# Performance work log

Hardware: AMD Instinct MI355X
Metric: run time of the kernel (lower is better)

The kernel has to match this reference:

```python
import jax, jax.numpy as jnp
import numpy as np

EPS = 1e-6

def _ln(x, g, b):
    m = jnp.mean(x, axis=-1, keepdims=True)
    v = jnp.mean(jnp.square(x - m), axis=-1, keepdims=True)
    return (x - m) * jax.lax.rsqrt(v + EPS) * g + b

def setup_inputs() -> dict:
    key = jax.random.key(0)
    ks = jax.random.split(key, 8)
    B, T, D, K = 512, 1024, 64, 16
    return {
        "z": jax.random.normal(ks[0], (B, T, D), jnp.float32),
        "prototypes": jax.random.normal(ks[1], (K, D), jnp.float32),
        "alphas": jax.random.normal(ks[2], (T, D), jnp.float32),
        "b_bias": jax.random.normal(ks[3], (D,), jnp.float32),
        "W": jax.random.normal(ks[4], (D, D), jnp.float32) / np.sqrt(D),
        "Wb": jax.random.normal(ks[5], (D,), jnp.float32) * 0.02,
        "ln_gamma": jnp.ones((5, D), jnp.float32),
        "ln_beta": jnp.zeros((5, D), jnp.float32),
        "beta_seq": jax.random.normal(ks[6], (K, D), jnp.float32) / np.sqrt(D),
    }

def reference(z, prototypes, alphas, b_bias, W, Wb, ln_gamma, ln_beta, beta_seq):
    # z: [B,T,D], prototypes: [K,D], alphas: [T,D]
    D = z.shape[-1]
    scale = 1.0 / jnp.sqrt(jnp.asarray(D, z.dtype))

    # --- intention_clustering: p_{k|i} ---
    zn = _ln(z, ln_gamma[0], ln_beta[0])                      # [B,T,D]
    pn = _ln(prototypes, ln_gamma[1], ln_beta[1])             # [K,D]
    scores_k = jnp.einsum('btd,kd->btk', zn, pn) * scale      # [B,T,K]
    p_k_i = jax.nn.softmax(scores_k, axis=-1)                 # normalize over intents K

    # --- intention_weighting: p_i ---
    k_ = _ln(alphas + z, ln_gamma[2], ln_beta[2])             # [B,T,D]
    k = k_ + jnp.einsum('btd,de->bte', k_, W) + Wb            # residual Dense
    q = _ln(alphas[-1] + z[:, -1] + b_bias, ln_gamma[3], ln_beta[3])  # [B,D] last-position query
    scores_t = jnp.einsum('btd,bd->bt', k, q) * scale         # [B,T]
    p_i = jax.nn.softmax(scores_t, axis=1)                    # normalize over positions T

    # --- intention_aggr ---
    w = p_k_i * p_i[..., None]                                # [B,T,K]
    out = jnp.einsum('btk,btd->bkd', w, z)                    # [B,K,D]
    return _ln(beta_seq + out, ln_gamma[4], ln_beta[4])       # [B,K,D]
```

## Files before the change

### kernel.cpp

```cpp
#include <hip/hip_runtime.h>
#include <math.h>

#define EPSF   1e-6f
#define SCALE  0.125f
#define NEG_HUGE -3.402823466e38f

#define PW_STRIDE 4104

__device__ __forceinline__ float rs_nr(float x) {
    float r = rsqrtf(x);
    return r * (1.5f - 0.5f * x * r * r);
}

__device__ __forceinline__ float dot4(float4 a, float4 b) {
    return fmaf(a.x, b.x, fmaf(a.y, b.y, fmaf(a.z, b.z, a.w * b.w)));
}

__device__ __forceinline__ float finish_token(
    float sz, float szz, float sa, float saa, float da,
    const float* dk, const float* s_sGP, const float* s_BP,
    float sG2Q, float TQc, float* sk, float* se)
{
    float m   = sz  * (1.f / 64.f);
    float var = szz * (1.f / 64.f) - m * m;
    float rs  = rs_nr(var + EPSF);
    float ma   = sa  * (1.f / 64.f);
    float vara = saa * (1.f / 64.f) - ma * ma;
    float rsa  = rs_nr(vara + EPSF);

    float st = (rsa * (da - ma * sG2Q) + TQc) * SCALE;

    float mx = NEG_HUGE;
#pragma unroll
    for (int k = 0; k < 16; ++k) {
        float s = (rs * (dk[k] - m * s_sGP[k]) + s_BP[k]) * SCALE;
        sk[k] = s;
        mx = fmaxf(mx, s);
    }
    float s0 = 0.f;
#pragma unroll
    for (int k = 0; k < 16; ++k) { sk[k] = __expf(sk[k] - mx); s0 += sk[k]; }
    *se = s0;
    return st;
}

extern "C" __global__ __launch_bounds__(512, 4)
void disent_encoder_kernel(const float* __restrict__ z,
                           const float* __restrict__ proto,
                           const float* __restrict__ alphas,
                           const float* __restrict__ b_bias,
                           const float* __restrict__ W,
                           const float* __restrict__ Wb,
                           const float* __restrict__ lng,
                           const float* __restrict__ lnb,
                           const float* __restrict__ beta_seq,
                           float* __restrict__ out)
{
    const int b    = blockIdx.x;
    const int tid  = threadIdx.x;
    const int lane = tid & 63;
    const int wid  = tid >> 6;

    __shared__ __align__(16) float s_pw[4 * PW_STRIDE];
    __shared__ __align__(16) float s_GP[16 * 64];
    __shared__ __align__(16) float s_G2Q[64];
    __shared__ float s_sGP[16];
    __shared__ float s_BP[16];
    __shared__ float s_red[12];
    __shared__ float s_c[2];

    const float* zb = z + (size_t)b * 1024 * 64;

    if (wid == 0) {
        int d = lane;
        float a = alphas[1023 * 64 + d] + zb[1023 * 64 + d] + b_bias[d];
        float s1 = a, s2 = a * a;
#pragma unroll
        for (int off = 32; off >= 1; off >>= 1) {
            s1 += __shfl_xor(s1, off);
            s2 += __shfl_xor(s2, off);
        }
        float m  = s1 * (1.f / 64.f);
        float v  = s2 * (1.f / 64.f) - m * m;
        float rs = rs_nr(v + EPSF);
        float qd = fmaf((a - m) * rs, lng[3*64 + d], lnb[3*64 + d]);
        float s = 0.f;
#pragma unroll 4
        for (int eq = 0; eq < 16; ++eq) {
            float4 w4 = *(const float4*)&W[d*64 + eq*4];
            s = fmaf(w4.x, __shfl(qd, 4*eq+0),
                fmaf(w4.y, __shfl(qd, 4*eq+1),
                fmaf(w4.z, __shfl(qd, 4*eq+2),
                fmaf(w4.w, __shfl(qd, 4*eq+3), s))));
        }
        float qpp  = qd + s;
        float G2Qd = lng[2*64 + d] * qpp;
        s_G2Q[d] = G2Qd;
        float r1 = G2Qd;
        float r2 = fmaf(lnb[2*64 + d], qpp, Wb[d] * qd);
#pragma unroll
        for (int off = 32; off >= 1; off >>= 1) {
            r1 += __shfl_xor(r1, off);
            r2 += __shfl_xor(r2, off);
        }
        if (d == 0) { s_c[0] = r1; s_c[1] = r2; }
    } else if (wid == 1 && lane < 16) {
        int k = lane;
        float s1 = 0.f, s2 = 0.f;
#pragma unroll 4
        for (int qd = 0; qd < 16; ++qd) {
            float4 p = *(const float4*)&proto[k*64 + qd*4];
            s1 += (p.x + p.y) + (p.z + p.w);
            s2 += dot4(p, p);
        }
        float m  = s1 * (1.f / 64.f);
        float v  = s2 * (1.f / 64.f) - m * m;
        float rs = rs_nr(v + EPSF);
        float sgp = 0.f, bp = 0.f;
        for (int d2 = 0; d2 < 64; ++d2) {
            float pn = fmaf((proto[k*64 + d2] - m) * rs, lng[64 + d2], lnb[64 + d2]);
            float gp = lng[d2] * pn;
            s_GP[k*64 + d2] = gp;
            sgp += gp;
            bp = fmaf(lnb[d2], pn, bp);
        }
        s_sGP[k] = sgp;
        s_BP[k]  = bp;
    }
    __syncthreads();

    const float sG2Q = s_c[0];
    const float TQc  = s_c[1];

    float st0, st1, se0, se1;
    float sk0[16], sk1[16];
    {
        const int t0 = tid;
        const float4* zp[2] = { (const float4*)(zb + (size_t)t0 * 64),
                                (const float4*)(zb + (size_t)(t0 + 512) * 64) };
        const float4* ap[2] = { (const float4*)(alphas + (size_t)t0 * 64),
                                (const float4*)(alphas + (size_t)(t0 + 512) * 64) };
        float dk[2][16];
#pragma unroll
        for (int k = 0; k < 16; ++k) { dk[0][k] = 0.f; dk[1][k] = 0.f; }
        float sz[2]  = {0.f, 0.f}, szz[2] = {0.f, 0.f};
        float sa[2]  = {0.f, 0.f}, saa[2] = {0.f, 0.f}, da[2] = {0.f, 0.f};

#pragma unroll 4
        for (int qd = 0; qd < 16; ++qd) {
            float4 gq = *(const float4*)&s_G2Q[qd*4];
            float4 zq[2], aq[2];
#pragma unroll
            for (int j = 0; j < 2; ++j) { zq[j] = zp[j][qd]; aq[j] = ap[j][qd]; }
#pragma unroll
            for (int j = 0; j < 2; ++j) {
                float ux = zq[j].x + aq[j].x, uy = zq[j].y + aq[j].y;
                float uz = zq[j].z + aq[j].z, uw = zq[j].w + aq[j].w;
                sz[j]  += (zq[j].x + zq[j].y) + (zq[j].z + zq[j].w);
                szz[j]  = fmaf(zq[j].x, zq[j].x, fmaf(zq[j].y, zq[j].y,
                          fmaf(zq[j].z, zq[j].z, fmaf(zq[j].w, zq[j].w, szz[j]))));
                sa[j]  += (ux + uy) + (uz + uw);
                saa[j]  = fmaf(ux, ux, fmaf(uy, uy, fmaf(uz, uz, fmaf(uw, uw, saa[j]))));
                da[j]   = fmaf(ux, gq.x, fmaf(uy, gq.y, fmaf(uz, gq.z, fmaf(uw, gq.w, da[j]))));
            }
#pragma unroll
            for (int k = 0; k < 16; ++k) {
                float4 g = *(const float4*)&s_GP[k*64 + qd*4];
#pragma unroll
                for (int j = 0; j < 2; ++j)
                    dk[j][k] = fmaf(zq[j].x, g.x, fmaf(zq[j].y, g.y,
                               fmaf(zq[j].z, g.z, fmaf(zq[j].w, g.w, dk[j][k]))));
            }
        }
        st0 = finish_token(sz[0], szz[0], sa[0], saa[0], da[0], dk[0],
                           s_sGP, s_BP, sG2Q, TQc, sk0, &se0);
        st1 = finish_token(sz[1], szz[1], sa[1], saa[1], da[1], dk[1],
                           s_sGP, s_BP, sG2Q, TQc, sk1, &se1);
    }

    float lm = fmaxf(st0, st1);
#pragma unroll
    for (int off = 32; off >= 1; off >>= 1) lm = fmaxf(lm, __shfl_xor(lm, off));
    if (lane == 0) s_red[wid] = lm;
    __syncthreads();
    if (tid == 0) {
        float m0 = s_red[0];
#pragma unroll
        for (int w = 1; w < 8; ++w) m0 = fmaxf(m0, s_red[w]);
        s_red[8] = m0;
    }
    __syncthreads();
    float M  = s_red[8];
    float e0 = __expf(st0 - M), e1 = __expf(st1 - M);
    float ls = e0 + e1;
#pragma unroll
    for (int off = 32; off >= 1; off >>= 1) ls += __shfl_xor(ls, off);
    if (lane == 0) s_red[wid] = ls;
    __syncthreads();
    if (tid == 0) {
        float s0 = 0.f;
#pragma unroll
        for (int w = 0; w < 8; ++w) s0 += s_red[w];
        s_red[9] = 1.f / s0;
    }
    __syncthreads();
    float invZ = s_red[9];

    {
        float c0 = (e0 * invZ) / se0;
        float c1 = (e1 * invZ) / se1;
        const int t0 = tid;
#pragma unroll
        for (int kq = 0; kq < 4; ++kq) {
            float4 w0 = make_float4(sk0[4*kq+0]*c0, sk0[4*kq+1]*c0,
                                    sk0[4*kq+2]*c0, sk0[4*kq+3]*c0);
            float4 w1 = make_float4(sk1[4*kq+0]*c1, sk1[4*kq+1]*c1,
                                    sk1[4*kq+2]*c1, sk1[4*kq+3]*c1);
            *(float4*)&s_pw[kq*PW_STRIDE + t0*4]         = w0;
            *(float4*)&s_pw[kq*PW_STRIDE + (t0 + 512)*4] = w1;
        }
    }
    __syncthreads();

    const int kq = lane >> 4;
    const int dq = lane & 15;
    float acc[4][4];
#pragma unroll
    for (int i = 0; i < 4; ++i)
#pragma unroll
        for (int j = 0; j < 4; ++j) acc[i][j] = 0.f;

    const int tb = wid * 128;
#pragma unroll 4
    for (int tt = 0; tt < 128; ++tt) {
        int t = tb + tt;
        float4 zq = *(const float4*)&zb[(size_t)t*64 + dq*4];
        float4 wq = *(const float4*)&s_pw[kq*PW_STRIDE + t*4];
        float zv[4] = { zq.x, zq.y, zq.z, zq.w };
        float wv[4] = { wq.x, wq.y, wq.z, wq.w };
#pragma unroll
        for (int i = 0; i < 4; ++i)
#pragma unroll
            for (int j = 0; j < 4; ++j)
                acc[i][j] = fmaf(wv[i], zv[j], acc[i][j]);
    }
    __syncthreads();

    float* s_part = s_pw;
#pragma unroll
    for (int i = 0; i < 4; ++i) {
        float4 v = make_float4(acc[i][0], acc[i][1], acc[i][2], acc[i][3]);
        *(float4*)&s_part[wid*1024 + (kq*4 + i)*64 + dq*4] = v;
    }
    __syncthreads();

    if (tid < 256) {
        int k  = tid >> 4;
        int dg = tid & 15;
        float4 v = make_float4(0.f, 0.f, 0.f, 0.f);
#pragma unroll
        for (int w = 0; w < 8; ++w) {
            float4 p = *(const float4*)&s_part[w*1024 + k*64 + dg*4];
            v.x += p.x; v.y += p.y; v.z += p.z; v.w += p.w;
        }
        float4 bs = *(const float4*)&beta_seq[k*64 + dg*4];
        v.x += bs.x; v.y += bs.y; v.z += bs.z; v.w += bs.w;

        float s1 = (v.x + v.y) + (v.z + v.w);
        float s2 = dot4(v, v);
#pragma unroll
        for (int off = 1; off <= 8; off <<= 1) {
            s1 += __shfl_xor(s1, off);
            s2 += __shfl_xor(s2, off);
        }
        float m   = s1 * (1.f / 64.f);
        float var = s2 * (1.f / 64.f) - m * m;
        float rs  = rs_nr(var + EPSF);
        float4 g4 = *(const float4*)&lng[4*64 + dg*4];
        float4 b4 = *(const float4*)&lnb[4*64 + dg*4];
        float4 o;
        o.x = fmaf((v.x - m) * rs, g4.x, b4.x);
        o.y = fmaf((v.y - m) * rs, g4.y, b4.y);
        o.z = fmaf((v.z - m) * rs, g4.z, b4.z);
        o.w = fmaf((v.w - m) * rs, g4.w, b4.w);
        *(float4*)&out[((size_t)b*16 + k)*64 + dg*4] = o;
    }
}

extern "C" void kernel_launch(void* const* d_in, const int* in_sizes, int n_in,
                              void* d_out, int out_size, void* d_ws, size_t ws_size,
                              hipStream_t stream) {
    const float* z        = (const float*)d_in[0];
    const float* proto    = (const float*)d_in[1];
    const float* alphas   = (const float*)d_in[2];
    const float* b_bias   = (const float*)d_in[3];
    const float* W        = (const float*)d_in[4];
    const float* Wb       = (const float*)d_in[5];
    const float* lng      = (const float*)d_in[6];
    const float* lnb      = (const float*)d_in[7];
    const float* beta_seq = (const float*)d_in[8];
    float* out = (float*)d_out;

    disent_encoder_kernel<<<dim3(512), dim3(512), 0, stream>>>(
        z, proto, alphas, b_bias, W, Wb, lng, lnb, beta_seq, out);
}
```

Before: 254.8 us.

## Halve weight staging buffer by processing token halves in two LDS passes

The per-token weight staging buffer in shared memory is split into two sequential passes of 512 tokens each, halving its stride and footprint. Each pass writes one half's weights, synchronises, and accumulates against the matching half of z. The aim is a smaller LDS allocation per block, which may allow more resident blocks per CU. The cost is extra barriers, and the later partial-sum reuse of s_pw may now have less room than before.

```diff
diff --git a/kernel.cpp b/kernel.cpp
--- a/kernel.cpp
+++ b/kernel.cpp
@@ -5,7 +5,7 @@
 #define SCALE  0.125f
 #define NEG_HUGE -3.402823466e38f
 
-#define PW_STRIDE 4104
+#define PW_STRIDE 2056
 
 __device__ __forceinline__ float rs_nr(float x) {
     float r = rsqrtf(x);
@@ -205,22 +205,8 @@
     }
     __syncthreads();
     float invZ = s_red[9];
-
-    {
-        float c0 = (e0 * invZ) / se0;
-        float c1 = (e1 * invZ) / se1;
-        const int t0 = tid;
-#pragma unroll
-        for (int kq = 0; kq < 4; ++kq) {
-            float4 w0 = make_float4(sk0[4*kq+0]*c0, sk0[4*kq+1]*c0,
-                                    sk0[4*kq+2]*c0, sk0[4*kq+3]*c0);
-            float4 w1 = make_float4(sk1[4*kq+0]*c1, sk1[4*kq+1]*c1,
-                                    sk1[4*kq+2]*c1, sk1[4*kq+3]*c1);
-            *(float4*)&s_pw[kq*PW_STRIDE + t0*4]         = w0;
-            *(float4*)&s_pw[kq*PW_STRIDE + (t0 + 512)*4] = w1;
-        }
-    }
-    __syncthreads();
+    const float c0 = (e0 * invZ) / se0;
+    const float c1 = (e1 * invZ) / se1;
 
     const int kq = lane >> 4;
     const int dq = lane & 15;
@@ -230,19 +216,53 @@
 #pragma unroll
         for (int j = 0; j < 4; ++j) acc[i][j] = 0.f;
 
-    const int tb = wid * 128;
-#pragma unroll 4
-    for (int tt = 0; tt < 128; ++tt) {
-        int t = tb + tt;
-        float4 zq = *(const float4*)&zb[(size_t)t*64 + dq*4];
-        float4 wq = *(const float4*)&s_pw[kq*PW_STRIDE + t*4];
-        float zv[4] = { zq.x, zq.y, zq.z, zq.w };
-        float wv[4] = { wq.x, wq.y, wq.z, wq.w };
-#pragma unroll
-        for (int i = 0; i < 4; ++i)
-#pragma unroll
-            for (int j = 0; j < 4; ++j)
-                acc[i][j] = fmaf(wv[i], zv[j], acc[i][j]);
+#pragma unroll
+    for (int kq2 = 0; kq2 < 4; ++kq2) {
+        float4 w0 = make_float4(sk0[4*kq2+0]*c0, sk0[4*kq2+1]*c0,
+                                sk0[4*kq2+2]*c0, sk0[4*kq2+3]*c0);
+        *(float4*)&s_pw[kq2*PW_STRIDE + tid*4] = w0;
+    }
+    __syncthreads();
+    {
+        const int tb = wid * 64;
+#pragma unroll 4
+        for (int tt = 0; tt < 64; ++tt) {
+            int t = tb + tt;
+            float4 zq = *(const float4*)&zb[(size_t)t*64 + dq*4];
+            float4 wq = *(const float4*)&s_pw[kq*PW_STRIDE + t*4];
+            float zv[4] = { zq.x, zq.y, zq.z, zq.w };
+            float wv[4] = { wq.x, wq.y, wq.z, wq.w };
+#pragma unroll
+            for (int i = 0; i < 4; ++i)
+#pragma unroll
+                for (int j = 0; j < 4; ++j)
+                    acc[i][j] = fmaf(wv[i], zv[j], acc[i][j]);
+        }
+    }
+    __syncthreads();
+
+#pragma unroll
+    for (int kq2 = 0; kq2 < 4; ++kq2) {
+        float4 w1 = make_float4(sk1[4*kq2+0]*c1, sk1[4*kq2+1]*c1,
+                                sk1[4*kq2+2]*c1, sk1[4*kq2+3]*c1);
+        *(float4*)&s_pw[kq2*PW_STRIDE + tid*4] = w1;
+    }
+    __syncthreads();
+    {
+        const int tb = wid * 64;
+#pragma unroll 4
+        for (int tt = 0; tt < 64; ++tt) {
+            int t = tb + tt;
+            float4 zq = *(const float4*)&zb[(size_t)(t + 512)*64 + dq*4];
+            float4 wq = *(const float4*)&s_pw[kq*PW_STRIDE + t*4];
+            float zv[4] = { zq.x, zq.y, zq.z, zq.w };
+            float wv[4] = { wq.x, wq.y, wq.z, wq.w };
+#pragma unroll
+            for (int i = 0; i < 4; ++i)
+#pragma unroll
+                for (int j = 0; j < 4; ++j)
+                    acc[i][j] = fmaf(wv[i], zv[j], acc[i][j]);
+        }
     }
     __syncthreads();
 
```

New measurement: 259.1 us. Within noise of the previous version (+1.7%).
